# Kernel optimization log

Hardware: AMD Instinct MI355X
Metric: run time of the kernel (lower is better)

The kernel has to match this reference:

```python
import jax, jax.numpy as jnp
import numpy as np

KERNEL_SIZE = 5
EPS = 1e-6


def setup_inputs() -> dict:
    key = jax.random.key(0)
    k1, k2 = jax.random.split(key)
    b, c, h, w = 16, 512, 64, 64
    hidden = 512
    input_dim = c + KERNEL_SIZE * KERNEL_SIZE  # 537
    x = jax.random.normal(k1, (b, c, h, w), dtype=jnp.float32)
    # 1x1 conv weight, stored as (out, in); kaiming-ish scale
    W = jax.random.normal(k2, (hidden, input_dim), dtype=jnp.float32) * (1.0 / np.sqrt(input_dim))
    bias = jnp.zeros((hidden,), dtype=jnp.float32)
    return {"x": x, "W": W, "bias": bias}


def spatial_descriptor(x, k):
    # x: (b,c,h,w) -> (b, k*k, h, w), local self-similarity (dot product) volume
    b, c, h, w = x.shape
    p = k // 2
    xp = jnp.pad(x, ((0, 0), (0, 0), (p, p), (p, p)))
    # small fixed loop over k*k offsets; each term is a fused multiply-reduce
    corrs = [
        jnp.sum(x * jax.lax.dynamic_slice(xp, (0, 0, di, dj), (b, c, h, w)), axis=1)
        for di in range(k)
        for dj in range(k)
    ]
    return jnp.stack(corrs, axis=1)  # (b, k*k, h, w)


def reference(x, W, bias):
    k = KERNEL_SIZE
    gs = spatial_descriptor(x, k)  # (b, k^2, h, w)
    # featureL2Norm over channel dim (note: eps added to sum-of-squares, then sqrt)
    norm = jnp.sqrt(jnp.sum(gs * gs, axis=1, keepdims=True) + EPS)
    gs = gs / norm
    feat = jnp.concatenate([x, gs], axis=1)  # (b, c+k^2, h, w)
    # 1x1 conv + ReLU
    out = jnp.einsum('bchw,oc->bohw', feat, W) + bias[None, :, None, None]
    return jax.nn.relu(out)
```

## Files before the change

kernel.cpp:

```cpp
#include <hip/hip_runtime.h>
#include <stdint.h>

#define C_IN 512
#define HW 4096
#define NPIX 65536
#define KPAD 544
#define KIN 537
#define HID 512

typedef __attribute__((ext_vector_type(8))) short bf16x8;
typedef __attribute__((ext_vector_type(4))) float f32x4;

__device__ __forceinline__ unsigned short f2bf(float f) {
  union { float f; uint32_t u; } v; v.f = f;
  uint32_t u = v.u;
  return (unsigned short)((u + 0x7fffu + ((u >> 16) & 1u)) >> 16);
}
__device__ __forceinline__ float bf2f(unsigned short h) {
  union { uint32_t u; float f; } v; v.u = ((uint32_t)h) << 16;
  return v.f;
}

__global__ void k_wconv(const float* __restrict__ W, unsigned short* __restrict__ Wb) {
  int idx = blockIdx.x * 256 + threadIdx.x;
  if (idx >= HID * KPAD) return;
  int o = idx / KPAD;
  int k = idx - o * KPAD;
  float v = (k < KIN) ? W[o * KIN + k] : 0.f;
  Wb[idx] = f2bf(v);
}

__device__ __forceinline__ int xelem(int sr, int sc, int kg) {
  return (sr * 20 + sc) * 64 + ((kg ^ (sc & 7)) * 8);
}

__global__ __launch_bounds__(256) void k_corr(const float* __restrict__ x,
                                              unsigned short* __restrict__ featB,
                                              unsigned short* __restrict__ part) {
  __shared__ unsigned short xt[8 * 20 * 64];
  int g = blockIdx.x;
  int bid = (g & 7) * 1024 + (g >> 3);
  int cs = bid & 7;
  int cg = (bid >> 3) & 3;
  int rg = (bid >> 5) & 15;
  int b  = bid >> 9;
  int t = threadIdx.x;
  int lane = t & 63;
  int w = t >> 6;
  int r0 = rg * 4, c0 = cg * 16;

  const float* xb = x + ((size_t)b * C_IN + cs * 64) * HW;

#pragma unroll
  for (int i = 0; i < 5; ++i) {
    int li = t + i * 256;
    int sc = li % 20;
    int t2 = li / 20;
    int kg = t2 >> 3, sr = t2 & 7;
    int ir = r0 - 2 + sr, ic = c0 - 2 + sc;
    unsigned short pk[8];
    if ((unsigned)ir < 64u && (unsigned)ic < 64u) {
      const float* src = xb + ir * 64 + ic;
#pragma unroll
      for (int j = 0; j < 8; ++j) pk[j] = f2bf(src[(kg * 8 + j) * HW]);
    } else {
#pragma unroll
      for (int j = 0; j < 8; ++j) pk[j] = 0;
    }
    *(bf16x8*)&xt[xelem(sr, sc, kg)] = *(bf16x8*)pk;
  }
  __syncthreads();

#pragma unroll
  for (int i = 0; i < 2; ++i) {
    int flat = t + i * 256;
    int px = flat >> 3, kg = flat & 7;
    int pr = px >> 4, pc = px & 15;
    int n = b * 4096 + (r0 + pr) * 64 + c0 + pc;
    *(bf16x8*)(featB + (size_t)n * KPAD + cs * 64 + kg * 8) =
        *(const bf16x8*)&xt[xelem(pr + 2, pc + 2, kg)];
  }

  int i15 = lane & 15;
  int tq = lane >> 4;
  int q = i15 - tq * 4;
  bool valid = (q >= 0) && (q < 4);

  bf16x8 afr[2];
#pragma unroll
  for (int ks = 0; ks < 2; ++ks)
    afr[ks] = *(const bf16x8*)&xt[xelem(w + 2, 2 + i15, ks * 4 + tq)];

  int nb = b * 4096 + (r0 + w) * 64 + c0;
#pragma unroll 1
  for (int di = 0; di < 5; ++di) {
    int sr = w + di;
    unsigned short* pbase = part + ((size_t)(cs * 25 + di * 5)) * NPIX + nb;
#pragma unroll
    for (int dj = 0; dj < 5; ++dj) {
      f32x4 acc = (f32x4){0.f, 0.f, 0.f, 0.f};
#pragma unroll
      for (int ks = 0; ks < 2; ++ks) {
        bf16x8 bfr = *(const bf16x8*)&xt[xelem(sr, dj + i15, ks * 4 + tq)];
        acc = __builtin_amdgcn_mfma_f32_16x16x32_bf16(afr[ks], bfr, acc, 0, 0, 0);
      }
      float val = (q == 0) ? acc[0]
                : (q == 1) ? acc[1]
                : (q == 2) ? acc[2] : acc[3];
      if (valid) pbase[(size_t)dj * NPIX + i15] = f2bf(val);
    }
  }
}

__global__ void k_norm(const unsigned short* __restrict__ part,
                       unsigned short* __restrict__ featB) {
  int n = blockIdx.x * 256 + threadIdx.x;
  float g[25];
  float ss = 0.f;
#pragma unroll
  for (int k = 0; k < 25; ++k) {
    float s = 0.f;
#pragma unroll
    for (int cs = 0; cs < 8; ++cs)
      s += bf2f(part[((size_t)cs * 25 + k) * NPIX + n]);
    g[k] = s;
    ss += s * s;
  }
  float inv = 1.0f / sqrtf(ss + 1e-6f);
  unsigned short buf[32];
#pragma unroll
  for (int k = 0; k < 25; ++k) buf[k] = f2bf(g[k] * inv);
#pragma unroll
  for (int k = 25; k < 32; ++k) buf[k] = 0;
#pragma unroll
  for (int j = 0; j < 4; ++j)
    *(bf16x8*)(featB + (size_t)n * KPAD + 512 + j * 8) = *(bf16x8*)&buf[j * 8];
}

typedef __attribute__((address_space(3))) unsigned int as3_uint;
typedef const __attribute__((address_space(1))) unsigned int as1_uint;

__device__ __forceinline__ void glds16(const void* g, void* l) {
  __builtin_amdgcn_global_load_lds((as1_uint*)g, (as3_uint*)l, 16, 0, 0);
}

__global__ __launch_bounds__(256) void k_gemm(const unsigned short* __restrict__ Wb,
                                              const unsigned short* __restrict__ featB,
                                              const float* __restrict__ bias,
                                              float* __restrict__ out) {
  __shared__ __attribute__((aligned(16))) unsigned short As[2][4096];
  __shared__ __attribute__((aligned(16))) unsigned short Bs[2][4096];
  int g = blockIdx.x;
  int bid = (g & 7) * 256 + (g >> 3);
  int mt = bid & 3;
  int nt = bid >> 2;
  int m0 = mt * 128;
  int n0 = nt * 128;
  int tid = threadIdx.x;
  int wave = tid >> 6;
  int lane = tid & 63;
  int wm = wave >> 1;
  int wn = wave & 1;
  int kg = lane >> 4;

  uint32_t aOff[4], bOff[4];
#pragma unroll
  for (int r = 0; r < 4; ++r) {
    int rr = wm * 64 + r * 16 + (lane & 15);
    aOff[r] = rr * 64 + ((kg ^ ((rr >> 1) & 3)) << 4);
  }
#pragma unroll
  for (int cb = 0; cb < 4; ++cb) {
    int rr = wn * 64 + cb * 16 + (lane & 15);
    bOff[cb] = rr * 64 + ((kg ^ ((rr >> 1) & 3)) << 4);
  }

  f32x4 acc[4][4];
#pragma unroll
  for (int r = 0; r < 4; ++r)
#pragma unroll
    for (int cb = 0; cb < 4; ++cb)
      acc[r][cb] = (f32x4){0.f, 0.f, 0.f, 0.f};

  auto STAGE = [&](int buf, int k0) {
#pragma unroll
    for (int qq = 0; qq < 2; ++qq) {
      int ci = wave * 2 + qq;
      int i = ci * 64 + lane;
      int rr = i >> 2;
      int slot = i & 3;
      int k8 = slot ^ ((rr >> 1) & 3);
      glds16(Wb + (size_t)(m0 + rr) * KPAD + k0 + k8 * 8, (char*)&As[buf][0] + ci * 1024);
      glds16(featB + (size_t)(n0 + rr) * KPAD + k0 + k8 * 8, (char*)&Bs[buf][0] + ci * 1024);
    }
  };

  STAGE(0, 0);
  __syncthreads();
  int cur = 0;
#pragma unroll 1
  for (int t = 0; t < 17; ++t) {
    if (t < 16) STAGE(cur ^ 1, (t + 1) * 32);
    const char* Ab = (const char*)&As[cur][0];
    const char* Bb = (const char*)&Bs[cur][0];
    bf16x8 af[4], bf[4];
#pragma unroll
    for (int r = 0; r < 4; ++r)
      af[r] = *(const bf16x8*)(Ab + aOff[r]);
#pragma unroll
    for (int cb = 0; cb < 4; ++cb)
      bf[cb] = *(const bf16x8*)(Bb + bOff[cb]);
#pragma unroll
    for (int cb = 0; cb < 4; ++cb)
#pragma unroll
      for (int r = 0; r < 4; ++r)
        acc[r][cb] = __builtin_amdgcn_mfma_f32_16x16x32_bf16(af[r], bf[cb], acc[r][cb], 0, 0, 0);
    __syncthreads();
    cur ^= 1;
  }

  int bb = n0 >> 12;
  int hwb = n0 & 4095;
  float* outb = out + (size_t)bb * (HID * HW) + hwb;
#pragma unroll
  for (int r = 0; r < 4; ++r) {
    int row0 = m0 + wm * 64 + r * 16 + (lane >> 4) * 4;
    float bv[4];
#pragma unroll
    for (int j = 0; j < 4; ++j) bv[j] = bias[row0 + j];
#pragma unroll
    for (int cb = 0; cb < 4; ++cb) {
      int col = wn * 64 + cb * 16 + (lane & 15);
#pragma unroll
      for (int j = 0; j < 4; ++j) {
        float v2 = acc[r][cb][j] + bv[j];
        v2 = fmaxf(v2, 0.f);
        outb[(size_t)(row0 + j) * HW + col] = v2;
      }
    }
  }
}

extern "C" void kernel_launch(void* const* d_in, const int* in_sizes, int n_in,
                              void* d_out, int out_size, void* d_ws, size_t ws_size,
                              hipStream_t stream) {
  const float* x = (const float*)d_in[0];
  const float* W = (const float*)d_in[1];
  const float* bias = (const float*)d_in[2];
  float* out = (float*)d_out;
  char* ws = (char*)d_ws;
  unsigned short* featB = (unsigned short*)ws;
  unsigned short* Wb = (unsigned short*)(ws + 71303168);
  unsigned short* part = (unsigned short*)(ws + 71860224);

  k_wconv<<<1088, 256, 0, stream>>>(W, Wb);
  k_corr<<<8192, 256, 0, stream>>>(x, featB, part);
  k_norm<<<256, 256, 0, stream>>>(part, featB);
  k_gemm<<<2048, 256, 0, stream>>>(Wb, featB, bias, out);
}
```

Before: 168.7 us.

## Split NCHW-to-bf16 transpose into its own kernel and feed corr from featB

Adds a k_xpose kernel that converts x to bf16 pixel-major featB through an LDS transpose, reading each channel row coalesced. k_corr now loads its halo tile from featB with 16-byte vector loads instead of strided fp32 gathers from x, and no longer writes featB itself. Both kernels get launch bounds requesting 8 blocks per SM. This removes the uncoalesced strided reads and the redundant halo conversion of fp32 x. In exchange it adds a kernel launch and an extra write-then-read pass over featB.

```diff
diff --git a/kernel.cpp b/kernel.cpp
--- a/kernel.cpp
+++ b/kernel.cpp
@@ -30,13 +30,37 @@
   Wb[idx] = f2bf(v);
 }
 
+__global__ __launch_bounds__(256, 8) void k_xpose(const float* __restrict__ x,
+                                                  unsigned short* __restrict__ featB) {
+  __shared__ unsigned short sm[64][70];
+  int g = blockIdx.x;
+  int b = g >> 9, cg = (g >> 6) & 7, pt = g & 63;
+  int c0 = cg * 64, p0 = pt * 64;
+  int t = threadIdx.x, lane = t & 63, w = t >> 6;
+  const float* xb = x + ((size_t)b * C_IN + c0) * HW + p0;
+#pragma unroll
+  for (int i = 0; i < 8; ++i) {
+    int ch = w * 16 + i * 2;
+    float a = xb[(size_t)ch * HW + lane];
+    float bq = xb[(size_t)(ch + 1) * HW + lane];
+    uint32_t pk = (uint32_t)f2bf(a) | ((uint32_t)f2bf(bq) << 16);
+    *(uint32_t*)&sm[lane][ch] = pk;
+  }
+  __syncthreads();
+#pragma unroll
+  for (int i = 0; i < 2; ++i) {
+    int px = (t >> 3) + i * 32, kg = t & 7;
+    int n = b * 4096 + p0 + px;
+    *(bf16x8*)(featB + (size_t)n * KPAD + c0 + kg * 8) = *(const bf16x8*)&sm[px][kg * 8];
+  }
+}
+
 __device__ __forceinline__ int xelem(int sr, int sc, int kg) {
   return (sr * 20 + sc) * 64 + ((kg ^ (sc & 7)) * 8);
 }
 
-__global__ __launch_bounds__(256) void k_corr(const float* __restrict__ x,
-                                              unsigned short* __restrict__ featB,
-                                              unsigned short* __restrict__ part) {
+__global__ __launch_bounds__(256, 8) void k_corr(const unsigned short* __restrict__ featB,
+                                                 unsigned short* __restrict__ part) {
   __shared__ unsigned short xt[8 * 20 * 64];
   int g = blockIdx.x;
   int bid = (g & 7) * 1024 + (g >> 3);
@@ -49,37 +73,26 @@
   int w = t >> 6;
   int r0 = rg * 4, c0 = cg * 16;
 
-  const float* xb = x + ((size_t)b * C_IN + cs * 64) * HW;
-
+  bf16x8 v[5];
+  int la[5];
 #pragma unroll
   for (int i = 0; i < 5; ++i) {
-    int li = t + i * 256;
-    int sc = li % 20;
-    int t2 = li / 20;
-    int kg = t2 >> 3, sr = t2 & 7;
+    int flat = t + i * 256;
+    int kg = flat & 7, pxi = flat >> 3;
+    int sc = pxi % 20, sr = pxi / 20;
     int ir = r0 - 2 + sr, ic = c0 - 2 + sc;
-    unsigned short pk[8];
+    la[i] = xelem(sr, sc, kg);
     if ((unsigned)ir < 64u && (unsigned)ic < 64u) {
-      const float* src = xb + ir * 64 + ic;
-#pragma unroll
-      for (int j = 0; j < 8; ++j) pk[j] = f2bf(src[(kg * 8 + j) * HW]);
+      int n = b * 4096 + ir * 64 + ic;
+      v[i] = *(const bf16x8*)(featB + (size_t)n * KPAD + cs * 64 + kg * 8);
     } else {
-#pragma unroll
-      for (int j = 0; j < 8; ++j) pk[j] = 0;
-    }
-    *(bf16x8*)&xt[xelem(sr, sc, kg)] = *(bf16x8*)pk;
-  }
+      v[i] = (bf16x8){0, 0, 0, 0, 0, 0, 0, 0};
+    }
+  }
+#pragma unroll
+  for (int i = 0; i < 5; ++i)
+    *(bf16x8*)&xt[la[i]] = v[i];
   __syncthreads();
-
-#pragma unroll
-  for (int i = 0; i < 2; ++i) {
-    int flat = t + i * 256;
-    int px = flat >> 3, kg = flat & 7;
-    int pr = px >> 4, pc = px & 15;
-    int n = b * 4096 + (r0 + pr) * 64 + c0 + pc;
-    *(bf16x8*)(featB + (size_t)n * KPAD + cs * 64 + kg * 8) =
-        *(const bf16x8*)&xt[xelem(pr + 2, pc + 2, kg)];
-  }
 
   int i15 = lane & 15;
   int tq = lane >> 4;
@@ -254,7 +267,8 @@
   unsigned short* part = (unsigned short*)(ws + 71860224);
 
   k_wconv<<<1088, 256, 0, stream>>>(W, Wb);
-  k_corr<<<8192, 256, 0, stream>>>(x, featB, part);
+  k_xpose<<<8192, 256, 0, stream>>>(x, featB);
+  k_corr<<<8192, 256, 0, stream>>>(featB, part);
   k_norm<<<256, 256, 0, stream>>>(part, featB);
   k_gemm<<<2048, 256, 0, stream>>>(Wb, featB, bias, out);
 }
```

After: 151.2 us. 1.12x faster.
